# Performance work log

Hardware: AMD Instinct MI355X
Metric: run time of the kernel (lower is better)

The kernel has to match this reference:

```python
import jax, jax.numpy as jnp
import numpy as np
from jax import lax

DEPTH = 5
LEAF = 2 ** DEPTH          # 32
GATES = LEAF - 1           # 31
LATENT = 128
IN_SHAPE = (128, 8, 8)     # C, H, W after mixture reshape
OUT_FEAT = IN_SHAPE[0] * IN_SHAPE[1] * IN_SHAPE[2]  # 8192
BATCH = 512


def conv_t(x, w, b):
    # PyTorch ConvTranspose2d(k=4, s=2, p=1): weight layout [in, out, kh, kw].
    # Equivalent fwd conv: flip spatial dims, swap in/out, lhs_dilation=2, pad k-1-p=2.
    w_ = jnp.flip(w, (2, 3)).transpose(1, 0, 2, 3)  # [out, in, kh, kw]
    y = lax.conv_general_dilated(
        x, w_, window_strides=(1, 1), padding=((2, 2), (2, 2)),
        lhs_dilation=(2, 2), dimension_numbers=("NCHW", "OIHW", "NCHW"))
    return y + b[None, :, None, None]


def leaf_probs_fn(x, gw, gb):
    # gatings: [B, GATES]
    g = jax.nn.sigmoid(x @ gw + gb)
    dens = jnp.ones((x.shape[0], 1), dtype=x.dtype)  # root density
    start = 0
    for d in range(1, DEPTH + 1):
        n_par = 2 ** (d - 1)
        gp = lax.dynamic_slice_in_dim(g, start, n_par, axis=1)  # [B, n_par]
        # left child (odd node index) uses g, right child uses 1-g, interleaved.
        dens = jnp.stack([dens * gp, dens * (1.0 - gp)], axis=-1).reshape(x.shape[0], 2 * n_par)
        start += n_par
    return dens  # [B, LEAF]


def setup_inputs() -> dict:
    key = jax.random.key(0)
    ks = jax.random.split(key, 10)
    C = IN_SHAPE[0]
    inp = {
        "x": jax.random.normal(ks[0], (BATCH, LATENT), dtype=jnp.float32),
        # SoftTree gating params (kaiming-normal ~ N(0, sqrt(2/fan_in)) approx)
        "gw": jax.random.normal(ks[1], (LATENT, GATES), dtype=jnp.float32) * (2.0 / LATENT) ** 0.5,
        "gb": jnp.zeros((GATES,), dtype=jnp.float32),
        # constant projection leaves
        "z": jax.random.normal(ks[2], (OUT_FEAT, LEAF), dtype=jnp.float32),
        # ConvTranspose2d weights, PyTorch layout [in_ch, out_ch, kh, kw]
        "w1": jax.random.normal(ks[3], (C, 128, 4, 4), dtype=jnp.float32) * 0.02,
        "b1": jnp.zeros((128,), dtype=jnp.float32),
        "w2": jax.random.normal(ks[4], (128, 64, 4, 4), dtype=jnp.float32) * 0.02,
        "b2": jnp.zeros((64,), dtype=jnp.float32),
        "w3": jax.random.normal(ks[5], (64, 3, 4, 4), dtype=jnp.float32) * 0.02,
        "b3": jnp.zeros((3,), dtype=jnp.float32),
    }
    return inp


def reference(x, gw, gb, z, w1, b1, w2, b2, w3, b3):
    lp = leaf_probs_fn(x, gw, gb)              # [B, LEAF]
    out = lp @ z.T                              # [B, OUT_FEAT] == (z @ lp.T).T
    out = out.reshape(-1, *IN_SHAPE)            # [B, 128, 8, 8]
    out = jax.nn.relu(conv_t(out, w1, b1))      # [B, 128, 16, 16]
    out = jax.nn.relu(conv_t(out, w2, b2))      # [B, 64, 32, 32]
    out = conv_t(out, w3, b3)                   # [B, 3, 64, 64]
    return out
```

## Files before the change

kernel.cpp:

```cpp
#include <hip/hip_runtime.h>
#include <hip/hip_bf16.h>
#include <stdint.h>

using bf16 = __hip_bfloat16;
typedef __attribute__((ext_vector_type(8))) short bf16x8;
typedef __attribute__((ext_vector_type(4))) float f32x4;

#define BATCHN 512

__device__ __forceinline__ void zero_halo_dev(bf16* buf, int H, int W, int C, int idx) {
  int nvec = C >> 3;
  int P = 2 * (W + 2) + 2 * H;
  if (idx >= BATCHN * P * nvec) return;
  int cv = idx % nvec;
  int p = (idx / nvec) % P;
  int b = idx / (nvec * P);
  int row, col;
  if (p < W + 2) { row = 0; col = p; }
  else if (p < 2 * (W + 2)) { row = H + 1; col = p - (W + 2); }
  else { int q = p - 2 * (W + 2); row = 1 + (q >> 1); col = (q & 1) ? (W + 1) : 0; }
  float4 z4 = {0.f, 0.f, 0.f, 0.f};
  *(float4*)(buf + ((size_t)(b * (H + 2) + row) * (W + 2) + col) * C + cv * 8) = z4;
}

__device__ __forceinline__ void wprep_dev(const float* w, bf16* wt, int IC, int OCr, int OCp, int idx) {
  int NC = IC / 32;
  if (idx >= 16 * OCp * IC) return;
  int e = idx & 7;
  int t = idx >> 3;
  int oc = t % OCp; t /= OCp;
  int q = t & 3; t >>= 2;
  int c = t % NC; t /= NC;
  int tap = t & 3, p = t >> 2;
  int ic = c * 32 + q * 8 + e;
  int dy = tap >> 1, dx = tap & 1;
  int py = p >> 1, px = p & 1;
  const int ktab[2][2] = {{1, 3}, {2, 0}};
  int ky = ktab[py][dy], kx = ktab[px][dx];
  float v = 0.f;
  if (oc < OCr) v = w[((ic * OCr + oc) * 4 + ky) * 4 + kx];
  wt[idx] = __float2bfloat16(v);
}

#define NB_Z1 1152
#define NB_Z2 2176
#define NB_Z3 2112
#define NB_W1 1024
#define NB_W2 512
#define NB_W3 64
#define NB_G  128

__global__ void prep_kernel(bf16* x1, bf16* x2, bf16* x3,
                            const float* w1, bf16* wt1, const float* w2, bf16* wt2,
                            const float* w3, bf16* wt3,
                            const float* x, const float* gw, const float* gb, float* lp) {
  int bid = blockIdx.x;
  int tid = threadIdx.x;
  if (bid < NB_Z1) { zero_halo_dev(x1, 8, 8, 128, bid * 256 + tid); return; }
  bid -= NB_Z1;
  if (bid < NB_Z2) { zero_halo_dev(x2, 16, 16, 128, bid * 256 + tid); return; }
  bid -= NB_Z2;
  if (bid < NB_Z3) { zero_halo_dev(x3, 32, 32, 64, bid * 256 + tid); return; }
  bid -= NB_Z3;
  if (bid < NB_W1) { wprep_dev(w1, wt1, 128, 128, 128, bid * 256 + tid); return; }
  bid -= NB_W1;
  if (bid < NB_W2) { wprep_dev(w2, wt2, 128, 64, 64, bid * 256 + tid); return; }
  bid -= NB_W2;
  if (bid < NB_W3) { wprep_dev(w3, wt3, 64, 3, 16, bid * 256 + tid); return; }
  bid -= NB_W3;
  __shared__ float xs[4][128];
  __shared__ float gs[4][32];
  const int sub = tid >> 6, t = tid & 63;
  const int b = bid * 4 + sub;
  xs[sub][t] = x[b * 128 + t];
  xs[sub][t + 64] = x[b * 128 + 64 + t];
  __syncthreads();
  if (t < 31) {
    float acc = gb[t];
    #pragma unroll 8
    for (int k = 0; k < 128; ++k) acc += xs[sub][k] * gw[k * 31 + t];
    gs[sub][t] = 1.f / (1.f + __expf(-acc));
  }
  __syncthreads();
  if (t < 32) {
    float prob = 1.f;
    #pragma unroll
    for (int d = 1; d <= 5; ++d) {
      int i = t >> (6 - d);
      int node = (1 << (d - 1)) - 1 + i;
      float gv = gs[sub][node];
      prob *= ((t >> (5 - d)) & 1) ? (1.f - gv) : gv;
    }
    lp[b * 32 + t] = prob;
  }
}

__global__ void mixture_kernel(const float* __restrict__ z, const float* __restrict__ lp,
                               bf16* __restrict__ x1) {
  __shared__ float lps[64 * 32];
  const int s = blockIdx.x;
  const int h = s >> 3, w = s & 7;
  const int b0 = blockIdx.y * 64;
  const int t = threadIdx.x;
  const int c = t & 127;
  const int half = t >> 7;
  float4 zr[8];
  const float4* zp = (const float4*)(z + (size_t)(c * 64 + s) * 32);
  #pragma unroll
  for (int i = 0; i < 8; ++i) zr[i] = zp[i];
  #pragma unroll
  for (int i = 0; i < 8; ++i) lps[t + 256 * i] = lp[b0 * 32 + t + 256 * i];
  __syncthreads();
  for (int bs = 0; bs < 32; ++bs) {
    int bl = half * 32 + bs;
    const float4* lr = (const float4*)(lps + bl * 32);
    float acc = 0.f;
    #pragma unroll
    for (int i = 0; i < 8; ++i) {
      float4 l4 = lr[i];
      acc += zr[i].x * l4.x + zr[i].y * l4.y + zr[i].z * l4.z + zr[i].w * l4.w;
    }
    int b = b0 + bl;
    x1[((size_t)(b * 10 + h + 1) * 10 + (w + 1)) * 128 + c] = __float2bfloat16(acc);
  }
}

template<int IC, int OCp, int OCr, int IH, int IW, int ROWS, int BN,
         int WAVES_M, int WAVES_N, int MI, int NI, bool RELU, bool FINAL>
__global__ __launch_bounds__(256, 2)
void convt_reg(const bf16* __restrict__ xin, const bf16* __restrict__ wt,
               const float* __restrict__ bias, bf16* __restrict__ xout,
               float* __restrict__ fout) {
  constexpr int NC = IC / 32;
  constexpr int PLANES = NC * 4;
  constexpr int IH2 = IH + 2, IW2 = IW + 2;
  constexpr int OH2 = 2 * IH + 2, OW2 = 2 * IW + 2;
  constexpr int NPIX = (ROWS + 2) * IW2;
  constexpr int BPI = IH / ROWS;
  constexpr int WM = MI * 16, WN = NI * 16;
  constexpr int LIW = (IW == 8 ? 3 : (IW == 16 ? 4 : 5));
  constexpr int ICV = IC / 8;
  __shared__ bf16 Alds[PLANES * NPIX * 8];

  const int tid = threadIdx.x;
  const int wave = tid >> 6, lane = tid & 63;
  const int q = lane >> 4, li = lane & 15;
  const int wm = wave / WAVES_N, wn = wave % WAVES_N;
  const int img = blockIdx.x / BPI;
  const int tb = blockIdx.x % BPI;
  const int n0 = blockIdx.y * BN;

  const bf16* src = xin + ((size_t)img * IH2 + tb * ROWS) * IW2 * IC;
  for (int g = tid; g < NPIX * ICV; g += 256) {
    const int pix = g / ICV;
    const int gr = g % ICV;
    const float4 v = *(const float4*)(src + (size_t)g * 8);
    *(float4*)(&Alds[(gr * NPIX + pix) * 8]) = v;
  }

  const bf16* wtp = wt + (size_t)(n0 + wn * WN + li) * 8;

  int cpix[MI];
  #pragma unroll
  for (int mi = 0; mi < MI; ++mi) {
    const int m = wm * WM + mi * 16 + li;
    cpix[mi] = ((m >> LIW) + 1) * IW2 + (m & (IW - 1)) + 1;
  }

  f32x4 acc[4][MI][NI];
  #pragma unroll
  for (int p = 0; p < 4; ++p)
    #pragma unroll
    for (int mi = 0; mi < MI; ++mi)
      #pragma unroll
      for (int nj = 0; nj < NI; ++nj)
        acc[p][mi][nj] = (f32x4){0.f, 0.f, 0.f, 0.f};

  bf16x8 bb[3][NC][NI];

  auto loadB = [&](int chunk, int buf) {
    #pragma unroll
    for (int c = 0; c < NC; ++c)
      #pragma unroll
      for (int nj = 0; nj < NI; ++nj)
        bb[buf][c][nj] = *(const bf16x8*)(wtp + ((size_t)(chunk * PLANES + c * 4 + q) * OCp + nj * 16) * 8);
  };
  auto compute = [&](int chunk, int buf) {
    const int p = chunk >> 2, tap = chunk & 3;
    const int py = p >> 1, px = p & 1;
    const int sh = ((tap >> 1) ? (py ? 1 : -1) * IW2 : 0) + ((tap & 1) ? (px ? 1 : -1) : 0);
    #pragma unroll
    for (int c = 0; c < NC; ++c) {
      #pragma unroll
      for (int mi = 0; mi < MI; ++mi) {
        const bf16x8 a = *(const bf16x8*)(Alds + ((c * 4 + q) * NPIX + cpix[mi] + sh) * 8);
        #pragma unroll
        for (int nj = 0; nj < NI; ++nj)
          acc[p][mi][nj] = __builtin_amdgcn_mfma_f32_16x16x32_bf16(a, bb[buf][c][nj], acc[p][mi][nj], 0, 0, 0);
      }
    }
  };

  loadB(0, 0);
  loadB(1, 1);
  __syncthreads();

  #pragma unroll
  for (int cc = 0; cc < 16; ++cc) {
    if (cc + 2 < 16) loadB(cc + 2, (cc + 2) % 3);
    compute(cc, cc % 3);
    if ((cc & 1) && cc < 15) __builtin_amdgcn_s_barrier();
  }

  if (!FINAL) {
    #pragma unroll
    for (int p = 0; p < 4; ++p) {
      const int py = p >> 1, px = p & 1;
      #pragma unroll
      for (int nj = 0; nj < NI; ++nj) {
        const int oc = n0 + wn * WN + nj * 16 + li;
        const float bv = bias[oc];
        #pragma unroll
        for (int mi = 0; mi < MI; ++mi) {
          #pragma unroll
          for (int r = 0; r < 4; ++r) {
            const int pix = (wm * MI + mi) * 16 + q * 4 + r;
            const int y = tb * ROWS + (pix >> LIW), x = pix & (IW - 1);
            float v = acc[p][mi][nj][r] + bv;
            if (RELU) v = fmaxf(v, 0.f);
            xout[(((size_t)img * OH2 + 2 * y + py + 1) * OW2 + 2 * x + px + 1) * OCp + oc] =
                __float2bfloat16(v);
          }
        }
      }
    }
  } else {
    const int oc = li;
    if (oc < OCr) {
      const float bv = bias[oc];
      #pragma unroll
      for (int py = 0; py < 2; ++py)
        #pragma unroll
        for (int mi = 0; mi < MI; ++mi)
          #pragma unroll
          for (int r = 0; r < 4; ++r) {
            const int pix = (wm * MI + mi) * 16 + q * 4 + r;
            const int y = tb * ROWS + (pix >> LIW), x = pix & (IW - 1);
            float2 v2;
            v2.x = acc[py * 2 + 0][mi][0][r] + bv;
            v2.y = acc[py * 2 + 1][mi][0][r] + bv;
            *(float2*)(&fout[(((size_t)img * 3 + oc) * 64 + 2 * y + py) * 64 + 2 * x]) = v2;
          }
    }
  }
}

extern "C" void kernel_launch(void* const* d_in, const int* in_sizes, int n_in,
                              void* d_out, int out_size, void* d_ws, size_t ws_size,
                              hipStream_t stream) {
  const float* x  = (const float*)d_in[0];
  const float* gw = (const float*)d_in[1];
  const float* gb = (const float*)d_in[2];
  const float* z  = (const float*)d_in[3];
  const float* w1 = (const float*)d_in[4];
  const float* b1 = (const float*)d_in[5];
  const float* w2 = (const float*)d_in[6];
  const float* b2 = (const float*)d_in[7];
  const float* w3 = (const float*)d_in[8];
  const float* b3 = (const float*)d_in[9];
  float* out = (float*)d_out;

  char* w = (char*)d_ws;
  float* lp  = (float*)(w);
  bf16* x1  = (bf16*)(w + 65536);
  bf16* x2  = (bf16*)(w + 13172736);
  bf16* x3  = (bf16*)(w + 55640064);
  bf16* wt1 = (bf16*)(w + 131399680);
  bf16* wt2 = (bf16*)(w + 131923968);
  bf16* wt3 = (bf16*)(w + 132186112);

  prep_kernel<<<NB_Z1 + NB_Z2 + NB_Z3 + NB_W1 + NB_W2 + NB_W3 + NB_G, 256, 0, stream>>>(
      x1, x2, x3, w1, wt1, w2, wt2, w3, wt3, x, gw, gb, lp);

  mixture_kernel<<<dim3(64, 8), 256, 0, stream>>>(z, lp, x1);

  convt_reg<128,128,128, 8, 8, 8, 64, 2,2, 2,2, true,false>
      <<<dim3(512, 2), 256, 0, stream>>>(x1, wt1, b1, x2, nullptr);
  convt_reg<128, 64, 64,16,16, 4, 64, 2,2, 2,2, true,false>
      <<<dim3(2048, 1), 256, 0, stream>>>(x2, wt2, b2, x3, nullptr);
  convt_reg< 64, 16,  3,32,32, 8, 16, 4,1, 4,1, false,true>
      <<<dim3(2048, 1), 256, 0, stream>>>(x3, wt3, b3, nullptr, out);
}
```

Before: 212.5 us.

## Switch transposed convs to 32x32x16 MFMA and share A loads across parity classes

Replaces the 16x16x32 MFMA conv kernel with a 32x32x16 bf16 MFMA version for the first two layers. The loop is reorganised over the nine distinct input shifts, so each LDS A-fragment is loaded once and reused by every output parity class that needs it. The weight layout is reordered to match the new K grouping, and the final layer gets its own kernel built the same way. This drops the register triple-buffered B prefetch and the barriers in favour of direct global weight loads per MFMA, and raises launch bounds to 3 blocks per CU, which may expose weight-load latency.

```diff
diff --git a/kernel.cpp b/kernel.cpp
--- a/kernel.cpp
+++ b/kernel.cpp
@@ -5,6 +5,7 @@
 using bf16 = __hip_bfloat16;
 typedef __attribute__((ext_vector_type(8))) short bf16x8;
 typedef __attribute__((ext_vector_type(4))) float f32x4;
+typedef __attribute__((ext_vector_type(16))) float f32x16;
 
 #define BATCHN 512
 
@@ -24,15 +25,14 @@
 }
 
 __device__ __forceinline__ void wprep_dev(const float* w, bf16* wt, int IC, int OCr, int OCp, int idx) {
-  int NC = IC / 32;
+  int KG = IC / 8;
   if (idx >= 16 * OCp * IC) return;
   int e = idx & 7;
   int t = idx >> 3;
   int oc = t % OCp; t /= OCp;
-  int q = t & 3; t >>= 2;
-  int c = t % NC; t /= NC;
+  int kg = t % KG; t /= KG;
   int tap = t & 3, p = t >> 2;
-  int ic = c * 32 + q * 8 + e;
+  int ic = kg * 8 + e;
   int dy = tap >> 1, dx = tap & 1;
   int py = p >> 1, px = p & 1;
   const int ktab[2][2] = {{1, 3}, {2, 0}};
@@ -125,30 +125,33 @@
   }
 }
 
-template<int IC, int OCp, int OCr, int IH, int IW, int ROWS, int BN,
-         int WAVES_M, int WAVES_N, int MI, int NI, bool RELU, bool FINAL>
-__global__ __launch_bounds__(256, 2)
-void convt_reg(const bf16* __restrict__ xin, const bf16* __restrict__ wt,
-               const float* __restrict__ bias, bf16* __restrict__ xout,
-               float* __restrict__ fout) {
-  constexpr int NC = IC / 32;
-  constexpr int PLANES = NC * 4;
+#define CLASS_TABLES \
+  constexpr int TAPA[9] = {0, 1, 1, 2, 2, 3, 3, 3, 3}; \
+  constexpr int DYA[9]  = {0, 0, 0,-1, 1,-1,-1, 1, 1}; \
+  constexpr int DXA[9]  = {0,-1, 1, 0, 0,-1, 1,-1, 1}; \
+  constexpr int MSK[9]  = {0xF,0x5,0xA,0x3,0xC,0x1,0x2,0x4,0x8};
+
+template<int IC, int OCp, int IH, int IW, int ROWS>
+__global__ __launch_bounds__(256, 3)
+void convt32(const bf16* __restrict__ xin, const bf16* __restrict__ wt,
+             const float* __restrict__ bias, bf16* __restrict__ xout) {
+  constexpr int KG = IC / 8;
+  constexpr int NS = IC / 16;
   constexpr int IH2 = IH + 2, IW2 = IW + 2;
   constexpr int OH2 = 2 * IH + 2, OW2 = 2 * IW + 2;
   constexpr int NPIX = (ROWS + 2) * IW2;
   constexpr int BPI = IH / ROWS;
-  constexpr int WM = MI * 16, WN = NI * 16;
-  constexpr int LIW = (IW == 8 ? 3 : (IW == 16 ? 4 : 5));
+  constexpr int LIW = (IW == 8 ? 3 : 4);
   constexpr int ICV = IC / 8;
-  __shared__ bf16 Alds[PLANES * NPIX * 8];
+  __shared__ bf16 Alds[KG * NPIX * 8];
 
   const int tid = threadIdx.x;
   const int wave = tid >> 6, lane = tid & 63;
-  const int q = lane >> 4, li = lane & 15;
-  const int wm = wave / WAVES_N, wn = wave % WAVES_N;
+  const int hl = lane >> 5, l32 = lane & 31;
+  const int wm = wave >> 1, wn = wave & 1;
   const int img = blockIdx.x / BPI;
   const int tb = blockIdx.x % BPI;
-  const int n0 = blockIdx.y * BN;
+  const int n0 = blockIdx.y * 64;
 
   const bf16* src = xin + ((size_t)img * IH2 + tb * ROWS) * IW2 * IC;
   for (int g = tid; g < NPIX * ICV; g += 256) {
@@ -158,100 +161,136 @@
     *(float4*)(&Alds[(gr * NPIX + pix) * 8]) = v;
   }
 
-  const bf16* wtp = wt + (size_t)(n0 + wn * WN + li) * 8;
+  const int m = wm * 32 + l32;
+  const int cpix = ((m >> LIW) + 1) * IW2 + (m & (IW - 1)) + 1;
+  const bf16* wtp = wt + (size_t)(n0 + wn * 32 + l32) * 8;
+
+  f32x16 acc[4];
+  #pragma unroll
+  for (int p = 0; p < 4; ++p)
+    #pragma unroll
+    for (int r = 0; r < 16; ++r) acc[p][r] = 0.f;
+
+  CLASS_TABLES
+  __syncthreads();
+
+  #pragma unroll
+  for (int e = 0; e < 9; ++e) {
+    const int tap = TAPA[e];
+    const int sh = (DYA[e] * IW2 + DXA[e]);
+    #pragma unroll
+    for (int s = 0; s < NS; ++s) {
+      const bf16x8 a = *(const bf16x8*)(Alds + (((s * 2 + hl) * NPIX) + cpix + sh) * 8);
+      #pragma unroll
+      for (int p = 0; p < 4; ++p) {
+        if (MSK[e] & (1 << p)) {
+          const int chunk = p * 4 + tap;
+          const bf16x8 b = *(const bf16x8*)(wtp + ((size_t)(chunk * KG + s * 2 + hl) * OCp) * 8);
+          acc[p] = __builtin_amdgcn_mfma_f32_32x32x16_bf16(a, b, acc[p], 0, 0, 0);
+        }
+      }
+    }
+  }
+
+  const int oc = n0 + wn * 32 + l32;
+  const float bv = bias[oc];
+  #pragma unroll
+  for (int p = 0; p < 4; ++p) {
+    const int py = p >> 1, px = p & 1;
+    #pragma unroll
+    for (int r = 0; r < 16; ++r) {
+      const int ml = wm * 32 + (r & 3) + 8 * (r >> 2) + 4 * hl;
+      const int y = tb * ROWS + (ml >> LIW), x = ml & (IW - 1);
+      float v = fmaxf(acc[p][r] + bv, 0.f);
+      xout[(((size_t)img * OH2 + 2 * y + py + 1) * OW2 + 2 * x + px + 1) * OCp + oc] =
+          __float2bfloat16(v);
+    }
+  }
+}
+
+__global__ __launch_bounds__(256, 3)
+void convt16_final(const bf16* __restrict__ xin, const bf16* __restrict__ wt,
+                   const float* __restrict__ bias, float* __restrict__ fout) {
+  constexpr int IC = 64, OCp = 16, OCr = 3, IH = 32, IW = 32, ROWS = 8;
+  constexpr int KG = IC / 8;
+  constexpr int NC = IC / 32;
+  constexpr int IH2 = IH + 2, IW2 = IW + 2;
+  constexpr int NPIX = (ROWS + 2) * IW2;
+  constexpr int BPI = IH / ROWS;
+  constexpr int MI = 4;
+  constexpr int ICV = IC / 8;
+  __shared__ bf16 Alds[KG * NPIX * 8];
+
+  const int tid = threadIdx.x;
+  const int wave = tid >> 6, lane = tid & 63;
+  const int q = lane >> 4, li = lane & 15;
+  const int img = blockIdx.x / BPI;
+  const int tb = blockIdx.x % BPI;
+
+  const bf16* src = xin + ((size_t)img * IH2 + tb * ROWS) * IW2 * IC;
+  for (int g = tid; g < NPIX * ICV; g += 256) {
+    const int pix = g / ICV;
+    const int gr = g % ICV;
+    const float4 v = *(const float4*)(src + (size_t)g * 8);
+    *(float4*)(&Alds[(gr * NPIX + pix) * 8]) = v;
+  }
 
   int cpix[MI];
   #pragma unroll
   for (int mi = 0; mi < MI; ++mi) {
-    const int m = wm * WM + mi * 16 + li;
-    cpix[mi] = ((m >> LIW) + 1) * IW2 + (m & (IW - 1)) + 1;
-  }
-
-  f32x4 acc[4][MI][NI];
+    const int m = wave * 64 + mi * 16 + li;
+    cpix[mi] = ((m >> 5) + 1) * IW2 + (m & 31) + 1;
+  }
+  const bf16* wtp = wt + (size_t)li * 8;
+
+  f32x4 acc[4][MI];
   #pragma unroll
   for (int p = 0; p < 4; ++p)
     #pragma unroll
     for (int mi = 0; mi < MI; ++mi)
+      acc[p][mi] = (f32x4){0.f, 0.f, 0.f, 0.f};
+
+  CLASS_TABLES
+  __syncthreads();
+
+  #pragma unroll
+  for (int e = 0; e < 9; ++e) {
+    const int tap = TAPA[e];
+    const int sh = (DYA[e] * IW2 + DXA[e]);
+    #pragma unroll
+    for (int c = 0; c < NC; ++c) {
+      bf16x8 bfr[4];
       #pragma unroll
-      for (int nj = 0; nj < NI; ++nj)
-        acc[p][mi][nj] = (f32x4){0.f, 0.f, 0.f, 0.f};
-
-  bf16x8 bb[3][NC][NI];
-
-  auto loadB = [&](int chunk, int buf) {
-    #pragma unroll
-    for (int c = 0; c < NC; ++c)
-      #pragma unroll
-      for (int nj = 0; nj < NI; ++nj)
-        bb[buf][c][nj] = *(const bf16x8*)(wtp + ((size_t)(chunk * PLANES + c * 4 + q) * OCp + nj * 16) * 8);
-  };
-  auto compute = [&](int chunk, int buf) {
-    const int p = chunk >> 2, tap = chunk & 3;
-    const int py = p >> 1, px = p & 1;
-    const int sh = ((tap >> 1) ? (py ? 1 : -1) * IW2 : 0) + ((tap & 1) ? (px ? 1 : -1) : 0);
-    #pragma unroll
-    for (int c = 0; c < NC; ++c) {
+      for (int p = 0; p < 4; ++p)
+        if (MSK[e] & (1 << p))
+          bfr[p] = *(const bf16x8*)(wtp + ((size_t)((p * 4 + tap) * KG + c * 4 + q) * OCp) * 8);
       #pragma unroll
       for (int mi = 0; mi < MI; ++mi) {
-        const bf16x8 a = *(const bf16x8*)(Alds + ((c * 4 + q) * NPIX + cpix[mi] + sh) * 8);
+        const bf16x8 a = *(const bf16x8*)(Alds + (((c * 4 + q) * NPIX) + cpix[mi] + sh) * 8);
         #pragma unroll
-        for (int nj = 0; nj < NI; ++nj)
-          acc[p][mi][nj] = __builtin_amdgcn_mfma_f32_16x16x32_bf16(a, bb[buf][c][nj], acc[p][mi][nj], 0, 0, 0);
+        for (int p = 0; p < 4; ++p)
+          if (MSK[e] & (1 << p))
+            acc[p][mi] = __builtin_amdgcn_mfma_f32_16x16x32_bf16(a, bfr[p], acc[p][mi], 0, 0, 0);
       }
     }
-  };
-
-  loadB(0, 0);
-  loadB(1, 1);
-  __syncthreads();
-
-  #pragma unroll
-  for (int cc = 0; cc < 16; ++cc) {
-    if (cc + 2 < 16) loadB(cc + 2, (cc + 2) % 3);
-    compute(cc, cc % 3);
-    if ((cc & 1) && cc < 15) __builtin_amdgcn_s_barrier();
-  }
-
-  if (!FINAL) {
-    #pragma unroll
-    for (int p = 0; p < 4; ++p) {
-      const int py = p >> 1, px = p & 1;
+  }
+
+  const int oc = li;
+  if (oc < OCr) {
+    const float bv = bias[oc];
+    #pragma unroll
+    for (int py = 0; py < 2; ++py)
       #pragma unroll
-      for (int nj = 0; nj < NI; ++nj) {
-        const int oc = n0 + wn * WN + nj * 16 + li;
-        const float bv = bias[oc];
+      for (int mi = 0; mi < MI; ++mi)
         #pragma unroll
-        for (int mi = 0; mi < MI; ++mi) {
-          #pragma unroll
-          for (int r = 0; r < 4; ++r) {
-            const int pix = (wm * MI + mi) * 16 + q * 4 + r;
-            const int y = tb * ROWS + (pix >> LIW), x = pix & (IW - 1);
-            float v = acc[p][mi][nj][r] + bv;
-            if (RELU) v = fmaxf(v, 0.f);
-            xout[(((size_t)img * OH2 + 2 * y + py + 1) * OW2 + 2 * x + px + 1) * OCp + oc] =
-                __float2bfloat16(v);
-          }
+        for (int r = 0; r < 4; ++r) {
+          const int pix = (wave * MI + mi) * 16 + q * 4 + r;
+          const int y = tb * ROWS + (pix >> 5), x = pix & 31;
+          float2 v2;
+          v2.x = acc[py * 2 + 0][mi][r] + bv;
+          v2.y = acc[py * 2 + 1][mi][r] + bv;
+          *(float2*)(&fout[(((size_t)img * 3 + oc) * 64 + 2 * y + py) * 64 + 2 * x]) = v2;
         }
-      }
-    }
-  } else {
-    const int oc = li;
-    if (oc < OCr) {
-      const float bv = bias[oc];
-      #pragma unroll
-      for (int py = 0; py < 2; ++py)
-        #pragma unroll
-        for (int mi = 0; mi < MI; ++mi)
-          #pragma unroll
-          for (int r = 0; r < 4; ++r) {
-            const int pix = (wm * MI + mi) * 16 + q * 4 + r;
-            const int y = tb * ROWS + (pix >> LIW), x = pix & (IW - 1);
-            float2 v2;
-            v2.x = acc[py * 2 + 0][mi][0][r] + bv;
-            v2.y = acc[py * 2 + 1][mi][0][r] + bv;
-            *(float2*)(&fout[(((size_t)img * 3 + oc) * 64 + 2 * y + py) * 64 + 2 * x]) = v2;
-          }
-    }
   }
 }
 
@@ -284,10 +323,7 @@
 
   mixture_kernel<<<dim3(64, 8), 256, 0, stream>>>(z, lp, x1);
 
-  convt_reg<128,128,128, 8, 8, 8, 64, 2,2, 2,2, true,false>
-      <<<dim3(512, 2), 256, 0, stream>>>(x1, wt1, b1, x2, nullptr);
-  convt_reg<128, 64, 64,16,16, 4, 64, 2,2, 2,2, true,false>
-      <<<dim3(2048, 1), 256, 0, stream>>>(x2, wt2, b2, x3, nullptr);
-  convt_reg< 64, 16,  3,32,32, 8, 16, 4,1, 4,1, false,true>
-      <<<dim3(2048, 1), 256, 0, stream>>>(x3, wt3, b3, nullptr, out);
-}
+  convt32<128, 128, 8, 8, 8><<<dim3(512, 2), 256, 0, stream>>>(x1, wt1, b1, x2);
+  convt32<128, 64, 16, 16, 4><<<dim3(2048, 1), 256, 0, stream>>>(x2, wt2, b2, x3);
+  convt16_final<<<dim3(2048, 1), 256, 0, stream>>>(x3, wt3, b3, out);
+}
```

New measurement: 218.5 us. 1.03x slower.
